# Kernel tuning notes

Measured on AMD Instinct MI355X. Metric: run time of the kernel, lower is better.

Reference implementation:

```python
import jax, jax.numpy as jnp
import numpy as np

N_NODES = 100000
N_EDGES = 1600000
IN_C, HID_C, OUT_C = 64, 64, 32


def setup_inputs() -> dict:
    key = jax.random.key(0)
    ks = jax.random.split(key, 6)
    x = jax.random.normal(ks[0], (N_NODES, IN_C), dtype=jnp.float32)
    edge_index = jax.random.randint(ks[1], (2, N_EDGES), 0, N_NODES, dtype=jnp.int64)
    edge_weight = jax.random.uniform(ks[2], (N_EDGES,), dtype=jnp.float32)
    # Glorot-ish init for the two GCNConv weight matrices, zero bias (PyG default)
    W1 = jax.random.normal(ks[3], (IN_C, HID_C), dtype=jnp.float32) / np.sqrt(IN_C)
    b1 = jnp.zeros((HID_C,), dtype=jnp.float32)
    W2 = jax.random.normal(ks[4], (HID_C, OUT_C), dtype=jnp.float32) / np.sqrt(HID_C)
    b2 = jnp.zeros((OUT_C,), dtype=jnp.float32)
    return {"x": x, "edge_index": edge_index, "edge_weight": edge_weight,
            "W1": W1, "b1": b1, "W2": W2, "b2": b2}


def _gcn_conv(x, src, dst, w, W, b):
    """PyG GCNConv: add self-loops (weight 1), symmetric D^-1/2 (A+I) D^-1/2 norm,
    then aggregate transformed features into destination nodes, plus bias."""
    n = x.shape[0]
    loop = jnp.arange(n, dtype=src.dtype)
    s = jnp.concatenate([src, loop])
    d = jnp.concatenate([dst, loop])
    wl = jnp.concatenate([w, jnp.ones((n,), dtype=x.dtype)])
    deg = jax.ops.segment_sum(wl, d, num_segments=n)            # [N]
    dinv = jnp.where(deg > 0, jax.lax.rsqrt(deg), 0.0)
    norm = dinv[s] * wl * dinv[d]                               # [E+N]
    xw = x @ W                                                  # [N, C_out]
    msg = norm[:, None] * xw[s]                                 # gather + scale
    return jax.ops.segment_sum(msg, d, num_segments=n) + b      # scatter-add


def reference(x, edge_index, edge_weight, W1, b1, W2, b2):
    src, dst = edge_index[0], edge_index[1]
    h = _gcn_conv(x, src, dst, edge_weight, W1, b1)
    h = jax.nn.relu(h)
    # dropout(p=0.5, training=self.training): identity in eval mode
    return _gcn_conv(h, src, dst, edge_weight, W2, b2)
```

## Files before the change

### kernel.cpp

```cpp
#include <hip/hip_runtime.h>

#define N_NODES 100000
#define N_EDGES 1600000
#define IN_C 64
#define HID_C 64
#define OUT_C 32

#define NB 391
#define BSHIFT 8
#define BMASK 255
#define SEG_CAP 4864
#define EPB 6272
#define BIN_BLOCKS ((N_EDGES + EPB - 1) / EPB)
#define G1_BLOCKS ((N_NODES + 63) / 64)
#define SMASK 0x1FFFF
#define FIXSCALE 34359738368.0f

__device__ __forceinline__ unsigned int bpack(float a, float b) {
    unsigned int ua = __float_as_uint(a);
    ua += 0x7FFFu + ((ua >> 16) & 1u);
    unsigned int ub = __float_as_uint(b);
    ub += 0x7FFFu + ((ub >> 16) & 1u);
    return (ua >> 16) | (ub & 0xFFFF0000u);
}
__device__ __forceinline__ float2 bup(unsigned int v) {
    return make_float2(__uint_as_float(v << 16), __uint_as_float(v & 0xFFFF0000u));
}


struct BinSh {
    int meta[EPB];
    int hist[NB];
    int gbase[NB];
};
struct G1Sh {
    float XsT[64][64];
    float Ws[64][64];
};
union FusedSh { BinSh b; G1Sh g; };

__global__ void __launch_bounds__(256) fused1_kernel(
    const int* __restrict__ src, const int* __restrict__ dst,
    const float* __restrict__ w, int* __restrict__ gcnt, int2* __restrict__ seg,
    const float* __restrict__ X, const float* __restrict__ W,
    unsigned int* __restrict__ XWu) {
    __shared__ FusedSh sh;
    int tid = threadIdx.x;
    if (blockIdx.x < BIN_BLOCKS) {
        for (int i = tid; i < NB; i += 256) sh.b.hist[i] = 0;
        __syncthreads();
        int e0 = blockIdx.x * EPB;
        int n = min(EPB, N_EDGES - e0);
        const int4* dst4 = (const int4*)(dst + e0);
        int n4 = n >> 2;
        for (int i = tid; i < n4; i += 256) {
            int4 d = dst4[i];
            int b0 = d.x >> BSHIFT, b1 = d.y >> BSHIFT;
            int b2 = d.z >> BSHIFT, b3 = d.w >> BSHIFT;
            sh.b.meta[0 * n4 + i] = atomicAdd(&sh.b.hist[b0], 1);
            sh.b.meta[1 * n4 + i] = atomicAdd(&sh.b.hist[b1], 1);
            sh.b.meta[2 * n4 + i] = atomicAdd(&sh.b.hist[b2], 1);
            sh.b.meta[3 * n4 + i] = atomicAdd(&sh.b.hist[b3], 1);
        }
        __syncthreads();
        for (int b = tid; b < NB; b += 256) {
            int c = sh.b.hist[b];
            sh.b.gbase[b] = c ? atomicAdd(&gcnt[b], c) : 0;
        }
        __syncthreads();
        const int4* src4 = (const int4*)(src + e0);
        const float4* w4 = (const float4*)(w + e0);
        for (int i = tid; i < n4; i += 256) {
            int4 s = src4[i];
            int4 d = dst4[i];
            float4 ww = w4[i];
#define FL_ONE(K, SS, DD, WW)                                              \
            {                                                              \
                int b = (DD) >> BSHIFT;                                    \
                int pos = sh.b.gbase[b] + sh.b.meta[K * n4 + i];           \
                if (pos < SEG_CAP)                                         \
                    seg[(size_t)b * SEG_CAP + pos] =                       \
                        make_int2((SS) | (((DD) & BMASK) << 17),           \
                                  __float_as_int(WW));                     \
            }
            FL_ONE(0, s.x, d.x, ww.x)
            FL_ONE(1, s.y, d.y, ww.y)
            FL_ONE(2, s.z, d.z, ww.z)
            FL_ONE(3, s.w, d.w, ww.w)
#undef FL_ONE
        }
    } else {
        {
            const float4* Wv = (const float4*)W;
            float4* Wsv = (float4*)&sh.g.Ws[0][0];
            for (int i = tid; i < 1024; i += 256) Wsv[i] = Wv[i];
        }
        int row0 = (blockIdx.x - BIN_BLOCKS) * 64;
        int rmax = N_NODES - row0;
        for (int i = tid; i < 64 * 16; i += 256) {
            int r = i & 63, kq = i >> 6;
            float4 v = (r < rmax) ? ((const float4*)(X + (size_t)(row0 + r) * IN_C))[kq]
                                  : make_float4(0.f, 0.f, 0.f, 0.f);
            sh.g.XsT[4 * kq + 0][r] = v.x;
            sh.g.XsT[4 * kq + 1][r] = v.y;
            sh.g.XsT[4 * kq + 2][r] = v.z;
            sh.g.XsT[4 * kq + 3][r] = v.w;
        }
        __syncthreads();
        int tr = tid >> 4, tc = tid & 15;
        float acc[4][4] = {};
        float a[4], bb[4];
#pragma unroll 8
        for (int k = 0; k < 64; ++k) {
            *(float4*)a = *(const float4*)&sh.g.XsT[k][4 * tr];
            *(float4*)bb = *(const float4*)&sh.g.Ws[k][4 * tc];
#pragma unroll
            for (int i = 0; i < 4; ++i)
#pragma unroll
                for (int j = 0; j < 4; ++j) acc[i][j] += a[i] * bb[j];
        }
#pragma unroll
        for (int i = 0; i < 4; ++i) {
            int rl = 4 * tr + i;
            if (rl < rmax) {
                int row = row0 + rl;
                uint2 o;
                o.x = bpack(acc[i][0], acc[i][1]);
                o.y = bpack(acc[i][2], acc[i][3]);
                ((uint2*)XWu)[(size_t)row * 16 + tc] = o;
            }
        }
    }
}


__global__ void __launch_bounds__(1024) bsort_kernel(const int* __restrict__ gcnt,
                                                     const int2* __restrict__ seg,
                                                     int2* __restrict__ seg2,
                                                     float* __restrict__ dinv,
                                                     int2* __restrict__ rowRC) {
    __shared__ unsigned long long packed[256];
    __shared__ int meta[SEG_CAP];
    __shared__ int sarr[256];
    __shared__ int ofs0[256];
    int tid = threadIdx.x, b = blockIdx.x;
    int n = min(gcnt[b], SEG_CAP);
    const int2* sp = seg + (size_t)b * SEG_CAP;
    if (tid < 256) packed[tid] = 0ULL;
    __syncthreads();
    for (int i = tid; i < n; i += 1024) {
        int2 r = sp[i];
        int dl = (r.x >> 17) & BMASK;
        unsigned long long fixw =
            (unsigned long long)(__int_as_float(r.y) * FIXSCALE);
        unsigned long long old = atomicAdd(&packed[dl], (1ULL << 48) | fixw);
        meta[i] = dl | ((int)(old >> 48) << 8);
    }
    __syncthreads();
    int myc = 0, padc = 0;
    if (tid < 256) {
        unsigned long long p = packed[tid];
        myc = (int)(p >> 48);
        float degw = (float)((double)(p & ((1ULL << 48) - 1)) * (1.0 / (double)FIXSCALE));
        float dv = rsqrtf(1.0f + degw);
        int node = (b << BSHIFT) + tid;
        if (node < N_NODES) dinv[node] = dv;
        padc = (myc + 1) & ~1;
        sarr[tid] = padc;
    }
    __syncthreads();
    for (int off = 1; off < 256; off <<= 1) {
        int tmp = 0;
        if (tid < 256 && tid >= off) tmp = sarr[tid - off];
        __syncthreads();
        if (tid < 256) sarr[tid] += tmp;
        __syncthreads();
    }
    if (tid < 256) {
        int excl = sarr[tid] - padc;
        int node = (b << BSHIFT) + tid;
        if (node < N_NODES) rowRC[node] = make_int2(b * SEG_CAP + excl, myc);
        ofs0[tid] = excl;
    }
    __syncthreads();
    int2* op = seg2 + (size_t)b * SEG_CAP;
    for (int i = tid; i < n; i += 1024) {
        int2 r = sp[i];
        int m = meta[i];
        int dl = m & BMASK, rank = m >> 8;
        op[ofs0[dl] + rank] = r;
    }
}


__global__ void __launch_bounds__(256) agg1_kernel(const int2* __restrict__ rowRC,
                                                   const int2* __restrict__ seg2,
                                                   const unsigned int* __restrict__ XWs,
                                                   const float* __restrict__ dinv,
                                                   const float* __restrict__ b1,
                                                   const float* __restrict__ W2,
                                                   unsigned int* __restrict__ HWs) {
    __shared__ float Hs[32][68];
    __shared__ float Ws2[64][32];
    int tid = threadIdx.x;
    {
        const float4* Wv = (const float4*)W2;
        float4* Wsv = (float4*)&Ws2[0][0];
        for (int i = tid; i < 512; i += 256) Wsv[i] = Wv[i];
    }
    int l8 = tid & 7;
    int nl = tid >> 3;
    int d = blockIdx.x * 32 + nl;
    const uint4* XW4 = (const uint4*)XWs;
    float did = dinv[d];
    float selfc = did * did;
    float4 bv0 = ((const float4*)b1)[2 * l8];
    float4 bv1 = ((const float4*)b1)[2 * l8 + 1];
    uint4 sv = XW4[(size_t)d * 8 + l8];
    float2 v;
    float a0, a1, a2, a3, a4, a5, a6, a7;
    v = bup(sv.x); a0 = bv0.x + selfc * v.x; a1 = bv0.y + selfc * v.y;
    v = bup(sv.y); a2 = bv0.z + selfc * v.x; a3 = bv0.w + selfc * v.y;
    v = bup(sv.z); a4 = bv1.x + selfc * v.x; a5 = bv1.y + selfc * v.y;
    v = bup(sv.w); a6 = bv1.z + selfc * v.x; a7 = bv1.w + selfc * v.y;
    int2 rc = rowRC[d];
    int nc = rc.y;
    const int2* sp = seg2 + rc.x;
    const int4* sp4 = (const int4*)sp;
    int e = 0;
#define ACC1(R, C)                                                         \
    v = bup(R.x); a0 += (C) * v.x; a1 += (C) * v.y;                        \
    v = bup(R.y); a2 += (C) * v.x; a3 += (C) * v.y;                        \
    v = bup(R.z); a4 += (C) * v.x; a5 += (C) * v.y;                        \
    v = bup(R.w); a6 += (C) * v.x; a7 += (C) * v.y;
    for (; e + 8 <= nc; e += 8) {
        int4 q0 = sp4[(e >> 1) + 0], q1 = sp4[(e >> 1) + 1];
        int4 q2 = sp4[(e >> 1) + 2], q3 = sp4[(e >> 1) + 3];
        int s0 = q0.x & SMASK, s1 = q0.z & SMASK, s2 = q1.x & SMASK, s3 = q1.z & SMASK;
        int s4 = q2.x & SMASK, s5 = q2.z & SMASK, s6 = q3.x & SMASK, s7 = q3.z & SMASK;
        float ds0 = dinv[s0], ds1 = dinv[s1], ds2 = dinv[s2], ds3 = dinv[s3];
        float ds4 = dinv[s4], ds5 = dinv[s5], ds6 = dinv[s6], ds7 = dinv[s7];
        uint4 r0 = XW4[(size_t)s0 * 8 + l8];
        uint4 r1 = XW4[(size_t)s1 * 8 + l8];
        uint4 r2 = XW4[(size_t)s2 * 8 + l8];
        uint4 r3 = XW4[(size_t)s3 * 8 + l8];
        uint4 r4 = XW4[(size_t)s4 * 8 + l8];
        uint4 r5 = XW4[(size_t)s5 * 8 + l8];
        uint4 r6 = XW4[(size_t)s6 * 8 + l8];
        uint4 r7 = XW4[(size_t)s7 * 8 + l8];
        float c0 = __int_as_float(q0.y) * did * ds0, c1 = __int_as_float(q0.w) * did * ds1;
        float c2 = __int_as_float(q1.y) * did * ds2, c3 = __int_as_float(q1.w) * did * ds3;
        float c4 = __int_as_float(q2.y) * did * ds4, c5 = __int_as_float(q2.w) * did * ds5;
        float c6 = __int_as_float(q3.y) * did * ds6, c7 = __int_as_float(q3.w) * did * ds7;
        ACC1(r0, c0) ACC1(r1, c1) ACC1(r2, c2) ACC1(r3, c3)
        ACC1(r4, c4) ACC1(r5, c5) ACC1(r6, c6) ACC1(r7, c7)
    }
    for (; e + 2 <= nc; e += 2) {
        int4 q = sp4[e >> 1];
        int s0 = q.x & SMASK, s1 = q.z & SMASK;
        float ds0 = dinv[s0], ds1 = dinv[s1];
        uint4 r0 = XW4[(size_t)s0 * 8 + l8];
        uint4 r1 = XW4[(size_t)s1 * 8 + l8];
        float c0 = __int_as_float(q.y) * did * ds0, c1 = __int_as_float(q.w) * did * ds1;
        ACC1(r0, c0) ACC1(r1, c1)
    }
    if (e < nc) {
        int2 p = sp[e];
        int s = p.x & SMASK;
        float c = __int_as_float(p.y) * did * dinv[s];
        uint4 r = XW4[(size_t)s * 8 + l8];
        ACC1(r, c)
    }
#undef ACC1
    *(float4*)&Hs[nl][8 * l8] = make_float4(fmaxf(a0, 0.f), fmaxf(a1, 0.f),
                                            fmaxf(a2, 0.f), fmaxf(a3, 0.f));
    *(float4*)&Hs[nl][8 * l8 + 4] = make_float4(fmaxf(a4, 0.f), fmaxf(a5, 0.f),
                                                fmaxf(a6, 0.f), fmaxf(a7, 0.f));
    __syncthreads();
    int nl2 = tid >> 3, cg = tid & 7;
    int d2 = blockIdx.x * 32 + nl2;
    float o0 = 0.f, o1 = 0.f, o2 = 0.f, o3 = 0.f;
#pragma unroll
    for (int k = 0; k < 64; ++k) {
        float hk = Hs[nl2][k];
        float4 wv = *(const float4*)&Ws2[k][4 * cg];
        o0 += hk * wv.x; o1 += hk * wv.y; o2 += hk * wv.z; o3 += hk * wv.w;
    }
    uint2 o;
    o.x = bpack(o0, o1);
    o.y = bpack(o2, o3);
    ((uint2*)HWs)[(size_t)d2 * 8 + cg] = o;
}


__global__ void __launch_bounds__(256) agg2_kernel(const int2* __restrict__ rowRC,
                                                   const int2* __restrict__ seg2,
                                                   const unsigned int* __restrict__ HWs,
                                                   const float* __restrict__ dinv,
                                                   const float* __restrict__ b2,
                                                   float* __restrict__ out) {
    int l4 = threadIdx.x & 3;
    int d = blockIdx.x * 64 + (threadIdx.x >> 2);
    if (d >= N_NODES) return;
    const uint4* HW4 = (const uint4*)HWs;
    float did = dinv[d];
    float selfc = did * did;
    float4 bv0 = ((const float4*)b2)[2 * l4];
    float4 bv1 = ((const float4*)b2)[2 * l4 + 1];
    uint4 sv = HW4[(size_t)d * 4 + l4];
    float2 v;
    float a0, a1, a2, a3, a4, a5, a6, a7;
    v = bup(sv.x); a0 = bv0.x + selfc * v.x; a1 = bv0.y + selfc * v.y;
    v = bup(sv.y); a2 = bv0.z + selfc * v.x; a3 = bv0.w + selfc * v.y;
    v = bup(sv.z); a4 = bv1.x + selfc * v.x; a5 = bv1.y + selfc * v.y;
    v = bup(sv.w); a6 = bv1.z + selfc * v.x; a7 = bv1.w + selfc * v.y;
    int2 rc = rowRC[d];
    int nc = rc.y;
    const int2* sp = seg2 + rc.x;
    const int4* sp4 = (const int4*)sp;
    int e = 0;
#define ACC2(R, C)                                                         \
    v = bup(R.x); a0 += (C) * v.x; a1 += (C) * v.y;                        \
    v = bup(R.y); a2 += (C) * v.x; a3 += (C) * v.y;                        \
    v = bup(R.z); a4 += (C) * v.x; a5 += (C) * v.y;                        \
    v = bup(R.w); a6 += (C) * v.x; a7 += (C) * v.y;
    for (; e + 8 <= nc; e += 8) {
        int4 q0 = sp4[(e >> 1) + 0], q1 = sp4[(e >> 1) + 1];
        int4 q2 = sp4[(e >> 1) + 2], q3 = sp4[(e >> 1) + 3];
        int s0 = q0.x & SMASK, s1 = q0.z & SMASK, s2 = q1.x & SMASK, s3 = q1.z & SMASK;
        int s4 = q2.x & SMASK, s5 = q2.z & SMASK, s6 = q3.x & SMASK, s7 = q3.z & SMASK;
        float ds0 = dinv[s0], ds1 = dinv[s1], ds2 = dinv[s2], ds3 = dinv[s3];
        float ds4 = dinv[s4], ds5 = dinv[s5], ds6 = dinv[s6], ds7 = dinv[s7];
        uint4 r0 = HW4[(size_t)s0 * 4 + l4];
        uint4 r1 = HW4[(size_t)s1 * 4 + l4];
        uint4 r2 = HW4[(size_t)s2 * 4 + l4];
        uint4 r3 = HW4[(size_t)s3 * 4 + l4];
        uint4 r4 = HW4[(size_t)s4 * 4 + l4];
        uint4 r5 = HW4[(size_t)s5 * 4 + l4];
        uint4 r6 = HW4[(size_t)s6 * 4 + l4];
        uint4 r7 = HW4[(size_t)s7 * 4 + l4];
        float c0 = __int_as_float(q0.y) * did * ds0, c1 = __int_as_float(q0.w) * did * ds1;
        float c2 = __int_as_float(q1.y) * did * ds2, c3 = __int_as_float(q1.w) * did * ds3;
        float c4 = __int_as_float(q2.y) * did * ds4, c5 = __int_as_float(q2.w) * did * ds5;
        float c6 = __int_as_float(q3.y) * did * ds6, c7 = __int_as_float(q3.w) * did * ds7;
        ACC2(r0, c0) ACC2(r1, c1) ACC2(r2, c2) ACC2(r3, c3)
        ACC2(r4, c4) ACC2(r5, c5) ACC2(r6, c6) ACC2(r7, c7)
    }
    for (; e + 2 <= nc; e += 2) {
        int4 q = sp4[e >> 1];
        int s0 = q.x & SMASK, s1 = q.z & SMASK;
        float ds0 = dinv[s0], ds1 = dinv[s1];
        uint4 r0 = HW4[(size_t)s0 * 4 + l4];
        uint4 r1 = HW4[(size_t)s1 * 4 + l4];
        float c0 = __int_as_float(q.y) * did * ds0, c1 = __int_as_float(q.w) * did * ds1;
        ACC2(r0, c0) ACC2(r1, c1)
    }
    if (e < nc) {
        int2 p = sp[e];
        int s = p.x & SMASK;
        float c = __int_as_float(p.y) * did * dinv[s];
        uint4 r = HW4[(size_t)s * 4 + l4];
        ACC2(r, c)
    }
#undef ACC2
    float4* o4 = (float4*)out + (size_t)d * 8 + l4 * 2;
    o4[0] = make_float4(a0, a1, a2, a3);
    o4[1] = make_float4(a4, a5, a6, a7);
}


extern "C" void kernel_launch(void* const* d_in, const int* in_sizes, int n_in,
                              void* d_out, int out_size, void* d_ws, size_t ws_size,
                              hipStream_t stream) {
    const float* x = (const float*)d_in[0];
    const int* edge_index = (const int*)d_in[1];
    const float* ew = (const float*)d_in[2];
    const float* W1 = (const float*)d_in[3];
    const float* b1 = (const float*)d_in[4];
    const float* W2 = (const float*)d_in[5];
    const float* b2 = (const float*)d_in[6];
    float* out = (float*)d_out;

    const int* src = edge_index;
    const int* dst = edge_index + N_EDGES;

    char* ws = (char*)d_ws;
    size_t off = 0;
    auto carve = [&](size_t bytes) -> void* {
        void* p = ws + off;
        off += (bytes + 255) & ~(size_t)255;
        return p;
    };

    int* gcnt = (int*)carve(NB * 4);
    float* dinv = (float*)carve((size_t)N_NODES * 4);
    int2* rowRC = (int2*)carve((size_t)N_NODES * 8);
    int2* seg = (int2*)carve((size_t)NB * SEG_CAP * 8);
    int2* seg2 = (int2*)carve((size_t)NB * SEG_CAP * 8);
    unsigned int* XWs = (unsigned int*)carve((size_t)N_NODES * 32 * 4);
    unsigned int* HWs = (unsigned int*)carve((size_t)N_NODES * 16 * 4);

    hipMemsetAsync(gcnt, 0, NB * 4, stream);
    fused1_kernel<<<BIN_BLOCKS + G1_BLOCKS, 256, 0, stream>>>(src, dst, ew, gcnt, seg,
                                                              x, W1, XWs);
    bsort_kernel<<<NB, 1024, 0, stream>>>(gcnt, seg, seg2, dinv, rowRC);
    agg1_kernel<<<N_NODES / 32, 256, 0, stream>>>(rowRC, seg2, XWs, dinv, b1, W2, HWs);
    agg2_kernel<<<(N_NODES + 63) / 64, 256, 0, stream>>>(rowRC, seg2, HWs, dinv, b2, out);
}
```

Before: 204.6 us.

## Split layer-2 features into channel slices and add nontemporal streaming loads/stores

```diff
diff --git a/kernel.cpp b/kernel.cpp
--- a/kernel.cpp
+++ b/kernel.cpp
@@ -16,6 +16,8 @@
 #define SMASK 0x1FFFF
 #define FIXSCALE 34359738368.0f
 
+#define A2_NB 782
+
 __device__ __forceinline__ unsigned int bpack(float a, float b) {
     unsigned int ua = __float_as_uint(a);
     ua += 0x7FFFu + ((ua >> 16) & 1u);
@@ -25,6 +27,21 @@
 }
 __device__ __forceinline__ float2 bup(unsigned int v) {
     return make_float2(__uint_as_float(v << 16), __uint_as_float(v & 0xFFFF0000u));
+}
+
+typedef int iv4 __attribute__((ext_vector_type(4)));
+typedef float fv4 __attribute__((ext_vector_type(4)));
+__device__ __forceinline__ int4 ntld(const int4* p) {
+    iv4 v = __builtin_nontemporal_load((const iv4*)p);
+    return make_int4(v.x, v.y, v.z, v.w);
+}
+__device__ __forceinline__ float4 ntldf(const float4* p) {
+    fv4 v = __builtin_nontemporal_load((const fv4*)p);
+    return make_float4(v.x, v.y, v.z, v.w);
+}
+__device__ __forceinline__ void ntst(float4* p, float4 s) {
+    fv4 t; t.x = s.x; t.y = s.y; t.z = s.z; t.w = s.w;
+    __builtin_nontemporal_store(t, (fv4*)p);
 }
 
 
@@ -71,9 +88,9 @@
         const int4* src4 = (const int4*)(src + e0);
         const float4* w4 = (const float4*)(w + e0);
         for (int i = tid; i < n4; i += 256) {
-            int4 s = src4[i];
+            int4 s = ntld(&src4[i]);
             int4 d = dst4[i];
-            float4 ww = w4[i];
+            float4 ww = ntldf(&w4[i]);
 #define FL_ONE(K, SS, DD, WW)                                              \
             {                                                              \
                 int b = (DD) >> BSHIFT;                                    \
@@ -99,7 +116,7 @@
         int rmax = N_NODES - row0;
         for (int i = tid; i < 64 * 16; i += 256) {
             int r = i & 63, kq = i >> 6;
-            float4 v = (r < rmax) ? ((const float4*)(X + (size_t)(row0 + r) * IN_C))[kq]
+            float4 v = (r < rmax) ? ntldf(&((const float4*)(X + (size_t)(row0 + r) * IN_C))[kq])
                                   : make_float4(0.f, 0.f, 0.f, 0.f);
             sh.g.XsT[4 * kq + 0][r] = v.x;
             sh.g.XsT[4 * kq + 1][r] = v.y;
@@ -234,8 +251,8 @@
     v = bup(R.z); a4 += (C) * v.x; a5 += (C) * v.y;                        \
     v = bup(R.w); a6 += (C) * v.x; a7 += (C) * v.y;
     for (; e + 8 <= nc; e += 8) {
-        int4 q0 = sp4[(e >> 1) + 0], q1 = sp4[(e >> 1) + 1];
-        int4 q2 = sp4[(e >> 1) + 2], q3 = sp4[(e >> 1) + 3];
+        int4 q0 = ntld(&sp4[(e >> 1) + 0]), q1 = ntld(&sp4[(e >> 1) + 1]);
+        int4 q2 = ntld(&sp4[(e >> 1) + 2]), q3 = ntld(&sp4[(e >> 1) + 3]);
         int s0 = q0.x & SMASK, s1 = q0.z & SMASK, s2 = q1.x & SMASK, s3 = q1.z & SMASK;
         int s4 = q2.x & SMASK, s5 = q2.z & SMASK, s6 = q3.x & SMASK, s7 = q3.z & SMASK;
         float ds0 = dinv[s0], ds1 = dinv[s1], ds2 = dinv[s2], ds3 = dinv[s3];
@@ -289,7 +306,7 @@
     uint2 o;
     o.x = bpack(o0, o1);
     o.y = bpack(o2, o3);
-    ((uint2*)HWs)[(size_t)d2 * 8 + cg] = o;
+    ((uint2*)HWs)[(size_t)(cg >> 2) * 400000 + (size_t)d2 * 4 + (cg & 3)] = o;
 }
 
 
@@ -299,15 +316,19 @@
                                                    const float* __restrict__ dinv,
                                                    const float* __restrict__ b2,
                                                    float* __restrict__ out) {
-    int l4 = threadIdx.x & 3;
-    int d = blockIdx.x * 64 + (threadIdx.x >> 2);
+    int bid = blockIdx.x;
+    int slice = (bid & 7) >> 2;
+    int nb = ((bid >> 3) << 2) | (bid & 3);
+    if (nb >= A2_NB) return;
+    int l2 = threadIdx.x & 1;
+    int d = nb * 128 + (threadIdx.x >> 1);
     if (d >= N_NODES) return;
-    const uint4* HW4 = (const uint4*)HWs;
+    const uint4* T = (const uint4*)HWs + (size_t)slice * 200000;
     float did = dinv[d];
     float selfc = did * did;
-    float4 bv0 = ((const float4*)b2)[2 * l4];
-    float4 bv1 = ((const float4*)b2)[2 * l4 + 1];
-    uint4 sv = HW4[(size_t)d * 4 + l4];
+    float4 bv0 = ((const float4*)b2)[slice * 4 + l2 * 2];
+    float4 bv1 = ((const float4*)b2)[slice * 4 + l2 * 2 + 1];
+    uint4 sv = T[(size_t)d * 2 + l2];
     float2 v;
     float a0, a1, a2, a3, a4, a5, a6, a7;
     v = bup(sv.x); a0 = bv0.x + selfc * v.x; a1 = bv0.y + selfc * v.y;
@@ -325,20 +346,20 @@
     v = bup(R.z); a4 += (C) * v.x; a5 += (C) * v.y;                        \
     v = bup(R.w); a6 += (C) * v.x; a7 += (C) * v.y;
     for (; e + 8 <= nc; e += 8) {
-        int4 q0 = sp4[(e >> 1) + 0], q1 = sp4[(e >> 1) + 1];
-        int4 q2 = sp4[(e >> 1) + 2], q3 = sp4[(e >> 1) + 3];
+        int4 q0 = ntld(&sp4[(e >> 1) + 0]), q1 = ntld(&sp4[(e >> 1) + 1]);
+        int4 q2 = ntld(&sp4[(e >> 1) + 2]), q3 = ntld(&sp4[(e >> 1) + 3]);
         int s0 = q0.x & SMASK, s1 = q0.z & SMASK, s2 = q1.x & SMASK, s3 = q1.z & SMASK;
         int s4 = q2.x & SMASK, s5 = q2.z & SMASK, s6 = q3.x & SMASK, s7 = q3.z & SMASK;
         float ds0 = dinv[s0], ds1 = dinv[s1], ds2 = dinv[s2], ds3 = dinv[s3];
         float ds4 = dinv[s4], ds5 = dinv[s5], ds6 = dinv[s6], ds7 = dinv[s7];
-        uint4 r0 = HW4[(size_t)s0 * 4 + l4];
-        uint4 r1 = HW4[(size_t)s1 * 4 + l4];
-        uint4 r2 = HW4[(size_t)s2 * 4 + l4];
-        uint4 r3 = HW4[(size_t)s3 * 4 + l4];
-        uint4 r4 = HW4[(size_t)s4 * 4 + l4];
-        uint4 r5 = HW4[(size_t)s5 * 4 + l4];
-        uint4 r6 = HW4[(size_t)s6 * 4 + l4];
-        uint4 r7 = HW4[(size_t)s7 * 4 + l4];
+        uint4 r0 = T[(size_t)s0 * 2 + l2];
+        uint4 r1 = T[(size_t)s1 * 2 + l2];
+        uint4 r2 = T[(size_t)s2 * 2 + l2];
+        uint4 r3 = T[(size_t)s3 * 2 + l2];
+        uint4 r4 = T[(size_t)s4 * 2 + l2];
+        uint4 r5 = T[(size_t)s5 * 2 + l2];
+        uint4 r6 = T[(size_t)s6 * 2 + l2];
+        uint4 r7 = T[(size_t)s7 * 2 + l2];
         float c0 = __int_as_float(q0.y) * did * ds0, c1 = __int_as_float(q0.w) * did * ds1;
         float c2 = __int_as_float(q1.y) * did * ds2, c3 = __int_as_float(q1.w) * did * ds3;
         float c4 = __int_as_float(q2.y) * did * ds4, c5 = __int_as_float(q2.w) * did * ds5;
@@ -350,8 +371,8 @@
         int4 q = sp4[e >> 1];
         int s0 = q.x & SMASK, s1 = q.z & SMASK;
         float ds0 = dinv[s0], ds1 = dinv[s1];
-        uint4 r0 = HW4[(size_t)s0 * 4 + l4];
-        uint4 r1 = HW4[(size_t)s1 * 4 + l4];
+        uint4 r0 = T[(size_t)s0 * 2 + l2];
+        uint4 r1 = T[(size_t)s1 * 2 + l2];
         float c0 = __int_as_float(q.y) * did * ds0, c1 = __int_as_float(q.w) * did * ds1;
         ACC2(r0, c0) ACC2(r1, c1)
     }
@@ -359,13 +380,13 @@
         int2 p = sp[e];
         int s = p.x & SMASK;
         float c = __int_as_float(p.y) * did * dinv[s];
-        uint4 r = HW4[(size_t)s * 4 + l4];
+        uint4 r = T[(size_t)s * 2 + l2];
         ACC2(r, c)
     }
 #undef ACC2
-    float4* o4 = (float4*)out + (size_t)d * 8 + l4 * 2;
-    o4[0] = make_float4(a0, a1, a2, a3);
-    o4[1] = make_float4(a4, a5, a6, a7);
+    float4* o4 = (float4*)out + (size_t)d * 8 + slice * 4 + l2 * 2;
+    ntst(o4, make_float4(a0, a1, a2, a3));
+    ntst(o4 + 1, make_float4(a4, a5, a6, a7));
 }
 
 
@@ -405,5 +426,5 @@
                                                               x, W1, XWs);
     bsort_kernel<<<NB, 1024, 0, stream>>>(gcnt, seg, seg2, dinv, rowRC);
     agg1_kernel<<<N_NODES / 32, 256, 0, stream>>>(rowRC, seg2, XWs, dinv, b1, W2, HWs);
-    agg2_kernel<<<(N_NODES + 63) / 64, 256, 0, stream>>>(rowRC, seg2, HWs, dinv, b2, out);
-}
+    agg2_kernel<<<1568, 256, 0, stream>>>(rowRC, seg2, HWs, dinv, b2, out);
+}
```

Measured after the change: 248.0 us. 1.21x slower.
